# Kernel optimization log

Hardware: AMD Instinct MI355X
Metric: run time of the kernel (lower is better)

Reference implementation:

```python
import jax, jax.numpy as jnp
import numpy as np
from jax import lax

BN_INV = float(1.0 / np.sqrt(1.0 + 1e-5))  # BatchNorm eval: running_mean=0, running_var=1


def _block(x, w, b, g, beta, stride):
    # Conv3x3(stride, pad=1) -> BN(eval) -> ReLU -> MaxPool2
    x = lax.conv_general_dilated(x, w, (stride, stride), [(1, 1), (1, 1)],
                                 dimension_numbers=('NCHW', 'OIHW', 'NCHW'))
    x = x + b[None, :, None, None]
    x = x * (g * BN_INV)[None, :, None, None] + beta[None, :, None, None]
    x = jax.nn.relu(x)
    return lax.reduce_window(x, -jnp.inf, lax.max, (1, 1, 2, 2), (1, 1, 2, 2), 'VALID')


def _gru(x, wi, wh, bi, bh):
    # torch-style GRU, batch_first. x: (B, T, D)
    B = x.shape[0]
    H = wh.shape[1]

    def step(h, xt):
        gi = xt @ wi.T + bi
        gh = h @ wh.T + bh
        ir, iz, inn = jnp.split(gi, 3, axis=1)
        hr, hz, hn = jnp.split(gh, 3, axis=1)
        r = jax.nn.sigmoid(ir + hr)
        z = jax.nn.sigmoid(iz + hz)
        nn_ = jnp.tanh(inn + r * hn)
        h2 = (1.0 - z) * nn_ + z * h
        return h2, h2

    h0 = jnp.zeros((B, H), x.dtype)
    _, ys = lax.scan(step, h0, jnp.swapaxes(x, 0, 1))
    return jnp.swapaxes(ys, 0, 1)  # (B, T, H)


def setup_inputs() -> dict:
    key = jax.random.key(0)
    ks = jax.random.split(key, 32)
    rn = lambda i, shape, s: jax.random.normal(ks[i], shape, jnp.float32) * s
    inp = {
        'support': rn(0, (5, 5, 1, 224, 224), 1.0),
        'query': rn(1, (15, 1, 224, 224), 1.0),
        'conv_w1': rn(2, (32, 1, 3, 3), 0.3), 'conv_b1': rn(3, (32,), 0.1),
        'conv_w2': rn(4, (64, 32, 3, 3), 0.06), 'conv_b2': rn(5, (64,), 0.1),
        'conv_w3': rn(6, (128, 64, 3, 3), 0.04), 'conv_b3': rn(7, (128,), 0.1),
        'conv_w4': rn(8, (256, 128, 3, 3), 0.03), 'conv_b4': rn(9, (256,), 0.1),
        'bn_g1': 1.0 + rn(10, (32,), 0.05), 'bn_be1': rn(11, (32,), 0.05),
        'bn_g2': 1.0 + rn(12, (64,), 0.05), 'bn_be2': rn(13, (64,), 0.05),
        'bn_g3': 1.0 + rn(14, (128,), 0.05), 'bn_be3': rn(15, (128,), 0.05),
        'bn_g4': 1.0 + rn(16, (256,), 0.05), 'bn_be4': rn(17, (256,), 0.05),
        'att_w': rn(18, (64, 256), 0.06), 'att_b': rn(19, (64,), 0.05),
        'gru_wi0': rn(20, (384, 512), 0.04), 'gru_wh0': rn(21, (384, 128), 0.08),
        'gru_bi0': rn(22, (384,), 0.05), 'gru_bh0': rn(23, (384,), 0.05),
        'gru_wi1': rn(24, (384, 128), 0.08), 'gru_wh1': rn(25, (384, 128), 0.08),
        'gru_bi1': rn(26, (384,), 0.05), 'gru_bh1': rn(27, (384,), 0.05),
        'trans_w': rn(28, (1, 128), 0.08), 'trans_b': rn(29, (1,), 0.05),
    }
    return inp


def reference(support, query, conv_w1, conv_b1, conv_w2, conv_b2, conv_w3, conv_b3,
              conv_w4, conv_b4, bn_g1, bn_be1, bn_g2, bn_be2, bn_g3, bn_be3,
              bn_g4, bn_be4, att_w, att_b, gru_wi0, gru_wh0, gru_bi0, gru_bh0,
              gru_wi1, gru_wh1, gru_bi1, gru_bh1, trans_w, trans_b):
    n, k, c, w = support.shape[0], support.shape[1], support.shape[2], support.shape[3]
    qk = query.shape[0]

    def enc(x):
        x = _block(x, conv_w1, conv_b1, bn_g1, bn_be1, 2)
        x = _block(x, conv_w2, conv_b2, bn_g2, bn_be2, 1)
        x = _block(x, conv_w3, conv_b3, bn_g3, bn_be3, 1)
        x = _block(x, conv_w4, conv_b4, bn_g4, bn_be4, 1)
        B, F_, H_, W_ = x.shape
        return x.reshape(B, F_, H_ * W_).transpose(0, 2, 1)  # (B, seq, feat)

    hf = enc(support.reshape(n * k, c, w, w))  # (nk, S, f)
    qf = enc(query)                            # (qk, T, f)

    # ItemQueryAttention: score[q,s,t,u] = sum_h tanh(W(q_t) * W(h_u))
    Wq = qf @ att_w.T + att_b  # (qk, T, h)
    Wh = hf @ att_w.T + att_b  # (nk, S, h)
    scores = jnp.tanh(Wq[:, None, :, None, :] * Wh[None, :, None, :, :]).sum(-1)  # (qk,nk,T,S)
    att = jax.nn.softmax(scores, axis=3)
    attended = jnp.einsum('qsTS,sSf->qsTf', att, hf)  # (qk, nk, T, f)

    T_, f = qf.shape[1], qf.shape[2]
    qrep = jnp.broadcast_to(qf[:, None], (qk, n * k, T_, f))
    x = jnp.concatenate([attended, qrep], axis=-1).reshape(qk * n * k, T_, 2 * f)

    h = _gru(x, gru_wi0, gru_wh0, gru_bi0, gru_bh0)
    h = _gru(h, gru_wi1, gru_wh1, gru_bi1, gru_bh1)

    logits = (h[:, -1, :] @ trans_w.T + trans_b).reshape(qk, n, k).sum(axis=2)  # (qk, n)
    return jax.nn.log_softmax(logits, axis=1)
```

## Files before the change

kernel.cpp:

```cpp
#include <hip/hip_runtime.h>
#include <hip/hip_bf16.h>
#include <math.h>

typedef unsigned short u16;
typedef unsigned int u32;
typedef __attribute__((ext_vector_type(8))) short bf16x8v;
typedef __attribute__((ext_vector_type(4))) float f32x4;

constexpr int NS = 25, NQ = 15, NB = 40;
constexpr int B3 = 375;
constexpr int T49 = 49;
constexpr float BN_INV = 0.9999950000374997f;

constexpr size_t A1H_OFF    = 0;
constexpr size_t A1L_OFF    = 8028160;
constexpr size_t X2_OFF     = 16056320;
constexpr size_t P2H_OFF    = 48168960;
constexpr size_t P2L_OFF    = 52183040;
constexpr size_t X3_OFF     = 0;
constexpr size_t P3H_OFF    = 56197120;
constexpr size_t P3L_OFF    = 58204160;
constexpr size_t X4_OFF     = 0;
constexpr size_t FEATTH_OFF = 60211200;
constexpr size_t FEATTL_OFF = 61214720;
constexpr size_t PROJ_OFF   = 0;
constexpr size_t ATTH_OFF   = 16056320;
constexpr size_t ATTL_OFF   = 25464320;
constexpr size_t GI_OFF     = 62218240;
constexpr size_t Y0H_OFF    = 0;
constexpr size_t Y0L_OFF    = 4704000;
constexpr size_t HFIN_OFF   = 90442240;
constexpr size_t WBH_OFF    = 91027456;
constexpr size_t WBL_OFF    = 92325888;
constexpr size_t W2_E = 0;
constexpr size_t W3_E = 18432;
constexpr size_t W4_E = 92160;
constexpr size_t AW_E = 387072;
constexpr size_t WI0_E = 403456;
constexpr size_t WI1_E = 600064;
constexpr int CVT_N = 649216;

static __device__ __forceinline__ u16 f2b(float f) {
  __hip_bfloat16 h = __float2bfloat16(f);
  return *reinterpret_cast<u16*>(&h);
}
static __device__ __forceinline__ float b2f(u16 u) {
  return __uint_as_float((u32)u << 16);
}
constexpr float LOG2E = 1.4426950408889634f;
static __device__ __forceinline__ float fsigmoid(float x) {
  return __builtin_amdgcn_rcpf(1.f + __builtin_amdgcn_exp2f(-x * LOG2E));
}
static __device__ __forceinline__ float ftanh(float x) {
  return 1.f - 2.f * __builtin_amdgcn_rcpf(__builtin_amdgcn_exp2f(x * (2.f * LOG2E)) + 1.f);
}
static __device__ __forceinline__ void split8(const float* v, u32* hp, u32* lp) {
  u16 h[8], l[8];
#pragma unroll
  for (int j = 0; j < 8; ++j) {
    const u16 hb = f2b(v[j]);
    h[j] = hb;
    l[j] = f2b(v[j] - b2f(hb));
  }
#pragma unroll
  for (int j = 0; j < 4; ++j) {
    hp[j] = (u32)h[2 * j] | ((u32)h[2 * j + 1] << 16);
    lp[j] = (u32)l[2 * j] | ((u32)l[2 * j + 1] << 16);
  }
}

__global__ void cvt_all(const float* __restrict__ cw2, const float* __restrict__ cw3,
                        const float* __restrict__ cw4, const float* __restrict__ aw,
                        const float* __restrict__ wi0, const float* __restrict__ wi1,
                        u16* __restrict__ oh, u16* __restrict__ ol) {
  const int i = blockIdx.x * 256 + threadIdx.x;
  if (i >= CVT_N) return;
  float v;
  if (i < (int)W3_E) {
    const int l = i, oc = l / 288, rem = l - oc * 288, e = rem >> 5, ic = rem & 31;
    v = cw2[((size_t)(oc * 32 + ic) * 3 + e / 3) * 3 + e % 3];
  } else if (i < (int)W4_E) {
    const int l = i - (int)W3_E, oc = l / 576, rem = l - oc * 576, e = rem >> 6, ic = rem & 63;
    v = cw3[((size_t)(oc * 64 + ic) * 3 + e / 3) * 3 + e % 3];
  } else if (i < (int)AW_E) {
    const int l = i - (int)W4_E, oc = l / 1152, rem = l - oc * 1152, e = rem >> 7, ic = rem & 127;
    v = cw4[((size_t)(oc * 128 + ic) * 3 + e / 3) * 3 + e % 3];
  } else if (i < (int)WI0_E) {
    v = aw[i - (int)AW_E];
  } else if (i < (int)WI1_E) {
    v = wi0[i - (int)WI0_E];
  } else {
    v = wi1[i - (int)WI1_E];
  }
  const u16 h = f2b(v);
  oh[i] = h;
  ol[i] = f2b(v - b2f(h));
}

__global__ __launch_bounds__(256) void conv1_pool(
    const float* __restrict__ support, const float* __restrict__ query,
    const float* __restrict__ w1, const float* __restrict__ cb1,
    const float* __restrict__ g1, const float* __restrict__ be1,
    u16* __restrict__ outh, u16* __restrict__ outl) {
  __shared__ float wl[288], scl[32], shl[32], cbl[32];
  const int tid = threadIdx.x;
  for (int l = tid; l < 288; l += 256) wl[l] = w1[l];
  if (tid < 32) { scl[tid] = g1[tid] * BN_INV; shl[tid] = be1[tid]; cbl[tid] = cb1[tid]; }
  __syncthreads();
  const int oc = tid & 31;
  const int p = blockIdx.x * 8 + (tid >> 5);
  const int ox = p % 56, oy = (p / 56) % 56, b = p / 3136;
  const float* in_b = (b < NS) ? (support + (size_t)b * 50176)
                               : (query + (size_t)(b - NS) * 50176);
  const int iy0 = 4 * oy - 1, ix0 = 4 * ox - 1;
  float pat[5][5];
#pragma unroll
  for (int dy = 0; dy < 5; ++dy) {
    const int iy = iy0 + dy;
#pragma unroll
    for (int dx = 0; dx < 5; ++dx) {
      const int ix = ix0 + dx;
      pat[dy][dx] = (iy >= 0 && iy < 224 && ix >= 0 && ix < 224)
                        ? in_b[(size_t)iy * 224 + ix] : 0.f;
    }
  }
  const float* wp = &wl[oc * 9];
  float mx = 0.f;
#pragma unroll
  for (int py = 0; py < 2; ++py)
#pragma unroll
    for (int px = 0; px < 2; ++px) {
      float acc = 0.f;
#pragma unroll
      for (int ky = 0; ky < 3; ++ky)
#pragma unroll
        for (int kx = 0; kx < 3; ++kx)
          acc += pat[2 * py + ky][2 * px + kx] * wp[ky * 3 + kx];
      float v = (acc + cbl[oc]) * scl[oc] + shl[oc];
      mx = fmaxf(mx, v);
    }
  const u16 h = f2b(mx);
  outh[(size_t)p * 32 + oc] = h;
  outl[(size_t)p * 32 + oc] = f2b(mx - b2f(h));
}

__global__ void maxpool2_split(const float* __restrict__ X, u16* __restrict__ Yh,
                               u16* __restrict__ Yl, int Bn, int H, int W, int C) {
  const int OH = H >> 1, OW = W >> 1;
  const int cpr = C >> 2;
  const int chunks = Bn * OH * OW * cpr;
  for (int i = blockIdx.x * blockDim.x + threadIdx.x; i < chunks;
       i += gridDim.x * blockDim.x) {
    const int c4 = i % cpr, m = i / cpr;
    const int ox = m % OW, oy = (m / OW) % OH, b = m / (OW * OH);
    const size_t base = (((size_t)b * H + 2 * oy) * W + 2 * ox) * C + (c4 << 2);
    const float4 r0 = *(const float4*)&X[base];
    const float4 r1 = *(const float4*)&X[base + C];
    const float4 r2 = *(const float4*)&X[base + (size_t)W * C];
    const float4 r3 = *(const float4*)&X[base + (size_t)W * C + C];
    float o[4];
    o[0] = fmaxf(fmaxf(r0.x, r1.x), fmaxf(r2.x, r3.x));
    o[1] = fmaxf(fmaxf(r0.y, r1.y), fmaxf(r2.y, r3.y));
    o[2] = fmaxf(fmaxf(r0.z, r1.z), fmaxf(r2.z, r3.z));
    o[3] = fmaxf(fmaxf(r0.w, r1.w), fmaxf(r2.w, r3.w));
    u16 hh[4], ll[4];
#pragma unroll
    for (int j = 0; j < 4; ++j) {
      hh[j] = f2b(o[j]);
      ll[j] = f2b(o[j] - b2f(hh[j]));
    }
    const size_t off = (size_t)m * C + (c4 << 2);
    uint2 vh, vl;
    vh.x = (u32)hh[0] | ((u32)hh[1] << 16); vh.y = (u32)hh[2] | ((u32)hh[3] << 16);
    vl.x = (u32)ll[0] | ((u32)ll[1] << 16); vl.y = (u32)ll[2] | ((u32)ll[3] << 16);
    *(uint2*)&Yh[off] = vh;
    *(uint2*)&Yl[off] = vl;
  }
}

template <int AMODE, int EPI>
__global__ __launch_bounds__(256) void sgemm(
    const u16* __restrict__ Ah, const u16* __restrict__ Al,
    const u16* __restrict__ A2h, const u16* __restrict__ A2l, int M, int K,
    const u16* __restrict__ Bh, const u16* __restrict__ Bl,
    const float* __restrict__ p0, const float* __restrict__ p1,
    const float* __restrict__ p2, float* __restrict__ Cout, int ldc,
    int H, int W, int IC, int icb) {
  __shared__ u16 Ash[64][72], Asl[64][72];
  __shared__ u16 Bsh[64][72], Bsl[64][72];
  const int tid = threadIdx.x;
  const int lane = tid & 63, wv = tid >> 6;
  const int wy = wv >> 1, wx = wv & 1;
  const int n0 = blockIdx.x * 64, m0 = blockIdx.y * 64;
  f32x4 acc[2][2] = {{{0, 0, 0, 0}, {0, 0, 0, 0}}, {{0, 0, 0, 0}, {0, 0, 0, 0}}};
  for (int k0 = 0; k0 < K; k0 += 64) {
#pragma unroll
    for (int s = 0; s < 2; ++s) {
      const int cc = s * 256 + tid;
      const int row = cc >> 3, kc = (cc & 7) << 3;
      const int gm = m0 + row, gk = k0 + kc;
      uint4 vh = {0u, 0u, 0u, 0u}, vl = {0u, 0u, 0u, 0u};
      if (AMODE == 0) {
        if (gm < M && gk < K) {
          const size_t idx = (size_t)gm * K + gk;
          vh = *(const uint4*)&Ah[idx];
          vl = *(const uint4*)&Al[idx];
        }
      } else if (AMODE == 1) {
        if (gm < M) {
          size_t idx;
          const u16 *ph_, *pl_;
          if (gk < 256) {
            idx = (size_t)gm * 256 + gk; ph_ = Ah; pl_ = Al;
          } else {
            const int b = gm / T49, t = gm % T49, q = b / NS;
            idx = (((size_t)(NS + q) * T49 + t) << 8) + (gk - 256);
            ph_ = A2h; pl_ = A2l;
          }
          vh = *(const uint4*)&ph_[idx];
          vl = *(const uint4*)&pl_[idx];
        }
      } else {
        if (gm < M && gk < K) {
          const int ox = gm % W, t_ = gm / W;
          const int oy = t_ % H, b = t_ / H;
          const int e = gk >> icb, ic = gk & (IC - 1);
          const int ky = e / 3, kx = e - 3 * (e / 3);
          const int iy = oy + ky - 1, ix = ox + kx - 1;
          if (iy >= 0 && iy < H && ix >= 0 && ix < W) {
            const size_t idx = (((size_t)b * H + iy) * W + ix) * IC + ic;
            vh = *(const uint4*)&Ah[idx];
            vl = *(const uint4*)&Al[idx];
          }
        }
      }
      *(uint4*)&Ash[row][kc] = vh;
      *(uint4*)&Asl[row][kc] = vl;
    }
#pragma unroll
    for (int s = 0; s < 2; ++s) {
      const int cc = s * 256 + tid;
      const int row = cc >> 3, kc = (cc & 7) << 3;
      const int gk = k0 + kc;
      uint4 vh = {0u, 0u, 0u, 0u}, vl = {0u, 0u, 0u, 0u};
      if (gk < K) {
        vh = *(const uint4*)&Bh[(size_t)(n0 + row) * K + gk];
        vl = *(const uint4*)&Bl[(size_t)(n0 + row) * K + gk];
      }
      *(uint4*)&Bsh[row][kc] = vh;
      *(uint4*)&Bsl[row][kc] = vl;
    }
    __syncthreads();
#pragma unroll
    for (int kk = 0; kk < 64; kk += 32) {
      const int ko = kk + ((lane >> 4) << 3);
      const int ra0 = wy * 32 + (lane & 15), ra1 = ra0 + 16;
      const int rb0 = wx * 32 + (lane & 15), rb1 = rb0 + 16;
      bf16x8v a0h = *(const bf16x8v*)&Ash[ra0][ko];
      bf16x8v a1h = *(const bf16x8v*)&Ash[ra1][ko];
      bf16x8v b0h = *(const bf16x8v*)&Bsh[rb0][ko];
      bf16x8v b1h = *(const bf16x8v*)&Bsh[rb1][ko];
      bf16x8v a0l = *(const bf16x8v*)&Asl[ra0][ko];
      bf16x8v a1l = *(const bf16x8v*)&Asl[ra1][ko];
      bf16x8v b0l = *(const bf16x8v*)&Bsl[rb0][ko];
      bf16x8v b1l = *(const bf16x8v*)&Bsl[rb1][ko];
      acc[0][0] = __builtin_amdgcn_mfma_f32_16x16x32_bf16(a0h, b0h, acc[0][0], 0, 0, 0);
      acc[0][1] = __builtin_amdgcn_mfma_f32_16x16x32_bf16(a0h, b1h, acc[0][1], 0, 0, 0);
      acc[1][0] = __builtin_amdgcn_mfma_f32_16x16x32_bf16(a1h, b0h, acc[1][0], 0, 0, 0);
      acc[1][1] = __builtin_amdgcn_mfma_f32_16x16x32_bf16(a1h, b1h, acc[1][1], 0, 0, 0);
      acc[0][0] = __builtin_amdgcn_mfma_f32_16x16x32_bf16(a0h, b0l, acc[0][0], 0, 0, 0);
      acc[0][1] = __builtin_amdgcn_mfma_f32_16x16x32_bf16(a0h, b1l, acc[0][1], 0, 0, 0);
      acc[1][0] = __builtin_amdgcn_mfma_f32_16x16x32_bf16(a1h, b0l, acc[1][0], 0, 0, 0);
      acc[1][1] = __builtin_amdgcn_mfma_f32_16x16x32_bf16(a1h, b1l, acc[1][1], 0, 0, 0);
      acc[0][0] = __builtin_amdgcn_mfma_f32_16x16x32_bf16(a0l, b0h, acc[0][0], 0, 0, 0);
      acc[0][1] = __builtin_amdgcn_mfma_f32_16x16x32_bf16(a0l, b1h, acc[0][1], 0, 0, 0);
      acc[1][0] = __builtin_amdgcn_mfma_f32_16x16x32_bf16(a1l, b0h, acc[1][0], 0, 0, 0);
      acc[1][1] = __builtin_amdgcn_mfma_f32_16x16x32_bf16(a1l, b1h, acc[1][1], 0, 0, 0);
    }
    __syncthreads();
  }
#pragma unroll
  for (int r = 0; r < 2; ++r) {
#pragma unroll
    for (int cI = 0; cI < 2; ++cI) {
      const int gn = n0 + wx * 32 + cI * 16 + (lane & 15);
      float sc0 = 0.f, sh0 = 0.f;
      if (EPI == 0) { sc0 = p1[gn] * BN_INV; sh0 = p2[gn]; }
#pragma unroll
      for (int i = 0; i < 4; ++i) {
        const int gm = m0 + wy * 32 + r * 16 + ((lane >> 4) << 2) + i;
        if (gm >= M) continue;
        const float a = acc[r][cI][i];
        if (EPI == 0) {
          Cout[(size_t)gm * ldc + gn] = fmaxf((a + p0[gn]) * sc0 + sh0, 0.f);
        } else {
          Cout[(size_t)gm * ldc + gn] = a + p0[gn];
        }
      }
    }
  }
}

__global__ __launch_bounds__(384) void attention_f32(
    const float* __restrict__ proj, const u16* __restrict__ featTh,
    const u16* __restrict__ featTl, u16* __restrict__ atth,
    u16* __restrict__ attl) {
  __shared__ float WqT[64][9];
  __shared__ float WhT[64][51];
  __shared__ float sc[7][64];
  const int bid = blockIdx.x;
  const int qs = bid / 7, tg = bid - 7 * qs;
  const int q = qs / NS, s = qs - NS * q;
  const int tid = threadIdx.x;
  const float* pq = proj + ((size_t)(NS + q) * T49 + tg * 7) * 64;
  const float* ph = proj + (size_t)s * T49 * 64;
  for (int l = tid; l < 7 * 64; l += 384) WqT[l & 63][l >> 6] = pq[l];
  for (int l = tid; l < T49 * 64; l += 384) WhT[l & 63][l >> 6] = ph[l];
  __syncthreads();
  constexpr float C2LOG2E = 2.8853900817779268f;
  if (tid < 343) {
    const int tl = tid / 49, u = tid - 49 * tl;
    float a0 = 0.f, a1 = 0.f, a2 = 0.f, a3 = 0.f;
#pragma unroll
    for (int h = 0; h < 64; h += 4) {
      const float p0 = WqT[h + 0][tl] * WhT[h + 0][u];
      const float p1 = WqT[h + 1][tl] * WhT[h + 1][u];
      const float p2 = WqT[h + 2][tl] * WhT[h + 2][u];
      const float p3 = WqT[h + 3][tl] * WhT[h + 3][u];
      a0 += 1.f - 2.f * __builtin_amdgcn_rcpf(__builtin_amdgcn_exp2f(p0 * C2LOG2E) + 1.f);
      a1 += 1.f - 2.f * __builtin_amdgcn_rcpf(__builtin_amdgcn_exp2f(p1 * C2LOG2E) + 1.f);
      a2 += 1.f - 2.f * __builtin_amdgcn_rcpf(__builtin_amdgcn_exp2f(p2 * C2LOG2E) + 1.f);
      a3 += 1.f - 2.f * __builtin_amdgcn_rcpf(__builtin_amdgcn_exp2f(p3 * C2LOG2E) + 1.f);
    }
    sc[tl][u] = (a0 + a1) + (a2 + a3);
  }
  __syncthreads();
  if (tid < 56) {
    const int t = tid >> 3, g = tid & 7;
    float m = -3.4e38f;
    for (int u = g; u < T49; u += 8) m = fmaxf(m, sc[t][u]);
    m = fmaxf(m, __shfl_xor(m, 4));
    m = fmaxf(m, __shfl_xor(m, 2));
    m = fmaxf(m, __shfl_xor(m, 1));
    float ssum = 0.f;
    for (int u = g; u < T49; u += 8) {
      const float e = __builtin_amdgcn_exp2f((sc[t][u] - m) * LOG2E);
      sc[t][u] = e; ssum += e;
    }
    ssum += __shfl_xor(ssum, 4);
    ssum += __shfl_xor(ssum, 2);
    ssum += __shfl_xor(ssum, 1);
    const float inv = 1.f / ssum;
    for (int u = g; u < T49; u += 8) sc[t][u] *= inv;
  }
  __syncthreads();
  if (tid < 256) {
    const u16* fsh = featTh + (size_t)s * T49 * 256;
    const u16* fsl = featTl + (size_t)s * T49 * 256;
    const size_t obase = ((size_t)qs * T49 + tg * 7) * 256;
    float acc[7] = {0.f, 0.f, 0.f, 0.f, 0.f, 0.f, 0.f};
    for (int u = 0; u < T49; ++u) {
      const float v = b2f(fsh[u * 256 + tid]) + b2f(fsl[u * 256 + tid]);
#pragma unroll
      for (int i = 0; i < 7; ++i) acc[i] += sc[i][u] * v;
    }
#pragma unroll
    for (int i = 0; i < 7; ++i) {
      const float a = acc[i];
      const u16 h = f2b(a);
      atth[obase + (size_t)i * 256 + tid] = h;
      attl[obase + (size_t)i * 256 + tid] = f2b(a - b2f(h));
    }
  }
}

constexpr int SPB = 8;
__global__ __launch_bounds__(512) void gru_mfma(
    const float* __restrict__ gi,
    const float* __restrict__ wh,
    const float* __restrict__ bh,
    u16* __restrict__ yh, u16* __restrict__ yl,
    float* __restrict__ hfin,
    int store_all) {
  __shared__ u16 hah[16][136];
  __shared__ float ghs[SPB][384];
  __shared__ float hfl[SPB][128];
  const int tid = threadIdx.x;
  const int lane = tid & 63, wv = tid >> 6;
  const int r0 = blockIdx.x * SPB;
  bf16x8v Bhr[3][4], Blr[3][4];
#pragma unroll
  for (int f = 0; f < 3; ++f) {
    const int n = (wv * 3 + f) * 16 + (lane & 15);
#pragma unroll
    for (int kk = 0; kk < 4; ++kk) {
      const int k = kk * 32 + ((lane >> 4) << 3);
      const float* p = wh + (size_t)n * 128 + k;
      float v[8];
      *(float4*)&v[0] = *(const float4*)p;
      *(float4*)&v[4] = *(const float4*)(p + 4);
      u32 hp[4], lp[4];
      split8(v, hp, lp);
      Bhr[f][kk] = *(bf16x8v*)hp;
      Blr[f][kk] = *(bf16x8v*)lp;
    }
  }
  const int row0 = tid >> 7, j0 = tid & 127;
  const int row1 = (512 + tid) >> 7, j1 = tid & 127;
  int sq0 = r0 + row0; if (sq0 >= B3) sq0 = B3 - 1;
  int sq1 = r0 + row1; if (sq1 >= B3) sq1 = B3 - 1;
  const float bhr0 = bh[j0], bhz0 = bh[128 + j0], bhn0 = bh[256 + j0];
  const float bhr1 = bh[j1], bhz1 = bh[128 + j1], bhn1 = bh[256 + j1];
  const float* gib0 = gi + (size_t)sq0 * T49 * 384;
  const float* gib1 = gi + (size_t)sq1 * T49 * 384;
  for (int i = tid; i < 16 * 136; i += 512) hah[i / 136][i % 136] = 0;
  for (int i = tid; i < SPB * 128; i += 512) hfl[i >> 7][i & 127] = 0.f;
  __syncthreads();
  const int ar = lane & 15, ko = (lane >> 4) << 3;
  float xr0c = gib0[j0], xz0c = gib0[128 + j0], xn0c = gib0[256 + j0];
  float xr1c = gib1[j1], xz1c = gib1[128 + j1], xn1c = gib1[256 + j1];
  for (int t = 0; t < T49; ++t) {
    const int tn = (t + 1 < T49) ? t + 1 : t;
    const float* g0n = gib0 + (size_t)tn * 384;
    const float* g1n = gib1 + (size_t)tn * 384;
    const float xr0n = g0n[j0], xz0n = g0n[128 + j0], xn0n = g0n[256 + j0];
    const float xr1n = g1n[j1], xz1n = g1n[128 + j1], xn1n = g1n[256 + j1];
    bf16x8v Ah[4];
#pragma unroll
    for (int kk = 0; kk < 4; ++kk)
      Ah[kk] = *(const bf16x8v*)&hah[ar][kk * 32 + ko];
#pragma unroll
    for (int f = 0; f < 3; ++f) {
      f32x4 acc = {0, 0, 0, 0};
#pragma unroll
      for (int kk = 0; kk < 4; ++kk)
        acc = __builtin_amdgcn_mfma_f32_16x16x32_bf16(Ah[kk], Bhr[f][kk], acc, 0, 0, 0);
#pragma unroll
      for (int kk = 0; kk < 4; ++kk)
        acc = __builtin_amdgcn_mfma_f32_16x16x32_bf16(Ah[kk], Blr[f][kk], acc, 0, 0, 0);
      const int nc = (wv * 3 + f) * 16 + (lane & 15);
      const int rb = (lane >> 4) << 2;
      if (rb < SPB) {
#pragma unroll
        for (int i = 0; i < 4; ++i) ghs[rb + i][nc] = acc[i];
      }
    }
    __syncthreads();
    {
      const float r_ = fsigmoid(xr0c + ghs[row0][j0] + bhr0);
      const float z_ = fsigmoid(xz0c + ghs[row0][128 + j0] + bhz0);
      const float n_ = ftanh(xn0c + r_ * (ghs[row0][256 + j0] + bhn0));
      const float hn = (1.f - z_) * n_ + z_ * hfl[row0][j0];
      hfl[row0][j0] = hn;
      const u16 hb = f2b(hn);
      hah[row0][j0] = hb;
      if (r0 + row0 < B3) {
        if (store_all) {
          const size_t o = ((size_t)(r0 + row0) * T49 + t) * 128 + j0;
          yh[o] = hb;
          yl[o] = f2b(hn - b2f(hb));
        } else if (t == T49 - 1) {
          hfin[(size_t)(r0 + row0) * 128 + j0] = hn;
        }
      }
    }
    {
      const float r_ = fsigmoid(xr1c + ghs[row1][j1] + bhr1);
      const float z_ = fsigmoid(xz1c + ghs[row1][128 + j1] + bhz1);
      const float n_ = ftanh(xn1c + r_ * (ghs[row1][256 + j1] + bhn1));
      const float hn = (1.f - z_) * n_ + z_ * hfl[row1][j1];
      hfl[row1][j1] = hn;
      const u16 hb = f2b(hn);
      hah[row1][j1] = hb;
      if (r0 + row1 < B3) {
        if (store_all) {
          const size_t o = ((size_t)(r0 + row1) * T49 + t) * 128 + j1;
          yh[o] = hb;
          yl[o] = f2b(hn - b2f(hb));
        } else if (t == T49 - 1) {
          hfin[(size_t)(r0 + row1) * 128 + j1] = hn;
        }
      }
    }
    __syncthreads();
    xr0c = xr0n; xz0c = xz0n; xn0c = xn0n;
    xr1c = xr1n; xz1c = xz1n; xn1c = xn1n;
  }
}

__global__ __launch_bounds__(512) void head_kernel(
    const float* __restrict__ hf, const float* __restrict__ tw,
    const float* __restrict__ tb, float* __restrict__ out) {
  __shared__ float lg[B3];
  const int tid = threadIdx.x;
  if (tid < B3) {
    const float* h = hf + (size_t)tid * 128;
    float acc = tb[0];
    for (int k = 0; k < 128; ++k) acc += h[k] * tw[k];
    lg[tid] = acc;
  }
  __syncthreads();
  if (tid < NQ) {
    float cls[5];
#pragma unroll
    for (int n = 0; n < 5; ++n) {
      float s = 0.f;
#pragma unroll
      for (int k = 0; k < 5; ++k) s += lg[tid * 25 + n * 5 + k];
      cls[n] = s;
    }
    float m = cls[0];
#pragma unroll
    for (int n = 1; n < 5; ++n) m = fmaxf(m, cls[n]);
    float se = 0.f;
#pragma unroll
    for (int n = 0; n < 5; ++n) se += expf(cls[n] - m);
    const float lse = m + logf(se);
#pragma unroll
    for (int n = 0; n < 5; ++n) out[tid * 5 + n] = cls[n] - lse;
  }
}

extern "C" void kernel_launch(void* const* d_in, const int* in_sizes, int n_in,
                              void* d_out, int out_size, void* d_ws,
                              size_t ws_size, hipStream_t stream) {
  (void)in_sizes; (void)n_in; (void)out_size; (void)ws_size;
  const float* support = (const float*)d_in[0];
  const float* query   = (const float*)d_in[1];
  const float* cw1 = (const float*)d_in[2];  const float* cb1 = (const float*)d_in[3];
  const float* cw2 = (const float*)d_in[4];  const float* cb2 = (const float*)d_in[5];
  const float* cw3 = (const float*)d_in[6];  const float* cb3 = (const float*)d_in[7];
  const float* cw4 = (const float*)d_in[8];  const float* cb4 = (const float*)d_in[9];
  const float* g1  = (const float*)d_in[10]; const float* be1 = (const float*)d_in[11];
  const float* g2  = (const float*)d_in[12]; const float* be2 = (const float*)d_in[13];
  const float* g3  = (const float*)d_in[14]; const float* be3 = (const float*)d_in[15];
  const float* g4  = (const float*)d_in[16]; const float* be4 = (const float*)d_in[17];
  const float* aw  = (const float*)d_in[18]; const float* ab  = (const float*)d_in[19];
  const float* wi0 = (const float*)d_in[20]; const float* wh0 = (const float*)d_in[21];
  const float* bi0 = (const float*)d_in[22]; const float* bh0 = (const float*)d_in[23];
  const float* wi1 = (const float*)d_in[24]; const float* wh1 = (const float*)d_in[25];
  const float* bi1 = (const float*)d_in[26]; const float* bh1 = (const float*)d_in[27];
  const float* tw  = (const float*)d_in[28]; const float* tb  = (const float*)d_in[29];

  char* ws = (char*)d_ws;
  float* out = (float*)d_out;
  u16* A1H    = (u16*)(ws + A1H_OFF);
  u16* A1L    = (u16*)(ws + A1L_OFF);
  float* X2   = (float*)(ws + X2_OFF);
  u16* P2H    = (u16*)(ws + P2H_OFF);
  u16* P2L    = (u16*)(ws + P2L_OFF);
  float* X3   = (float*)(ws + X3_OFF);
  u16* P3H    = (u16*)(ws + P3H_OFF);
  u16* P3L    = (u16*)(ws + P3L_OFF);
  float* X4   = (float*)(ws + X4_OFF);
  u16* FEATTH = (u16*)(ws + FEATTH_OFF);
  u16* FEATTL = (u16*)(ws + FEATTL_OFF);
  float* PROJ = (float*)(ws + PROJ_OFF);
  u16* ATTH   = (u16*)(ws + ATTH_OFF);
  u16* ATTL   = (u16*)(ws + ATTL_OFF);
  float* GI   = (float*)(ws + GI_OFF);
  u16* Y0H    = (u16*)(ws + Y0H_OFF);
  u16* Y0L    = (u16*)(ws + Y0L_OFF);
  float* HFIN = (float*)(ws + HFIN_OFF);
  u16* WBH = (u16*)(ws + WBH_OFF);
  u16* WBL = (u16*)(ws + WBL_OFF);

  cvt_all<<<(CVT_N + 255) / 256, 256, 0, stream>>>(cw2, cw3, cw4, aw, wi0, wi1, WBH, WBL);

  conv1_pool<<<15680, 256, 0, stream>>>(support, query, cw1, cb1, g1, be1, A1H, A1L);
  sgemm<2, 0><<<dim3(1, 1960), 256, 0, stream>>>(
      A1H, A1L, nullptr, nullptr, 125440, 288, WBH + W2_E, WBL + W2_E,
      cb2, g2, be2, X2, 64, 56, 56, 32, 5);
  maxpool2_split<<<1960, 256, 0, stream>>>(X2, P2H, P2L, NB, 56, 56, 64);
  sgemm<2, 0><<<dim3(2, 490), 256, 0, stream>>>(
      P2H, P2L, nullptr, nullptr, 31360, 576, WBH + W3_E, WBL + W3_E,
      cb3, g3, be3, X3, 128, 28, 28, 64, 6);
  maxpool2_split<<<980, 256, 0, stream>>>(X3, P3H, P3L, NB, 28, 28, 128);
  sgemm<2, 0><<<dim3(4, 123), 256, 0, stream>>>(
      P3H, P3L, nullptr, nullptr, 7840, 1152, WBH + W4_E, WBL + W4_E,
      cb4, g4, be4, X4, 256, 14, 14, 128, 7);
  maxpool2_split<<<490, 256, 0, stream>>>(X4, FEATTH, FEATTL, NB, 14, 14, 256);

  sgemm<0, 1><<<dim3(1, 31), 256, 0, stream>>>(
      FEATTH, FEATTL, nullptr, nullptr, NB * T49, 256, WBH + AW_E, WBL + AW_E,
      ab, nullptr, nullptr, PROJ, 64, 0, 0, 0, 0);
  attention_f32<<<B3 * 7, 384, 0, stream>>>(PROJ, FEATTH, FEATTL, ATTH, ATTL);

  sgemm<1, 1><<<dim3(6, 288), 256, 0, stream>>>(
      ATTH, ATTL, FEATTH, FEATTL, B3 * T49, 512, WBH + WI0_E, WBL + WI0_E,
      bi0, nullptr, nullptr, GI, 384, 0, 0, 0, 0);
  gru_mfma<<<47, 512, 0, stream>>>(GI, wh0, bh0, Y0H, Y0L, nullptr, 1);
  sgemm<0, 1><<<dim3(6, 288), 256, 0, stream>>>(
      Y0H, Y0L, nullptr, nullptr, B3 * T49, 128, WBH + WI1_E, WBL + WI1_E,
      bi1, nullptr, nullptr, GI, 384, 0, 0, 0, 0);
  gru_mfma<<<47, 512, 0, stream>>>(GI, wh1, bh1, nullptr, nullptr, HFIN, 0);

  head_kernel<<<1, 512, 0, stream>>>(HFIN, tw, tb, out);
}
```

Before: 368.6 us.

## Precompute query half of GRU input projection once per query and broadcast

Result: no change. 368.1 us (-0.1%).

```diff
diff --git a/kernel.cpp b/kernel.cpp
--- a/kernel.cpp
+++ b/kernel.cpp
@@ -24,6 +24,7 @@
 constexpr size_t FEATTH_OFF = 60211200;
 constexpr size_t FEATTL_OFF = 61214720;
 constexpr size_t PROJ_OFF   = 0;
+constexpr size_t QG_OFF     = 1048576;
 constexpr size_t ATTH_OFF   = 16056320;
 constexpr size_t ATTL_OFF   = 25464320;
 constexpr size_t GI_OFF     = 62218240;
@@ -31,14 +32,17 @@
 constexpr size_t Y0L_OFF    = 4704000;
 constexpr size_t HFIN_OFF   = 90442240;
 constexpr size_t WBH_OFF    = 91027456;
-constexpr size_t WBL_OFF    = 92325888;
+constexpr size_t WBL_OFF    = 92719104;
 constexpr size_t W2_E = 0;
 constexpr size_t W3_E = 18432;
 constexpr size_t W4_E = 92160;
 constexpr size_t AW_E = 387072;
 constexpr size_t WI0_E = 403456;
 constexpr size_t WI1_E = 600064;
-constexpr int CVT_N = 649216;
+constexpr int    CVT_N = 649216;
+constexpr size_t WI0A_E = 649216;
+constexpr size_t WI0B_E = 747520;
+constexpr int    CVT_N2 = 845824;
 
 static __device__ __forceinline__ u16 f2b(float f) {
   __hip_bfloat16 h = __float2bfloat16(f);
@@ -74,7 +78,7 @@
                         const float* __restrict__ wi0, const float* __restrict__ wi1,
                         u16* __restrict__ oh, u16* __restrict__ ol) {
   const int i = blockIdx.x * 256 + threadIdx.x;
-  if (i >= CVT_N) return;
+  if (i >= CVT_N2) return;
   float v;
   if (i < (int)W3_E) {
     const int l = i, oc = l / 288, rem = l - oc * 288, e = rem >> 5, ic = rem & 31;
@@ -89,8 +93,14 @@
     v = aw[i - (int)AW_E];
   } else if (i < (int)WI1_E) {
     v = wi0[i - (int)WI0_E];
+  } else if (i < CVT_N) {
+    v = wi1[i - (int)WI1_E];
+  } else if (i < (int)WI0B_E) {
+    const int l = i - (int)WI0A_E, j = l >> 8, k = l & 255;
+    v = wi0[(size_t)j * 512 + k];
   } else {
-    v = wi1[i - (int)WI1_E];
+    const int l = i - (int)WI0B_E, j = l >> 8, k = l & 255;
+    v = wi0[(size_t)j * 512 + 256 + k];
   }
   const u16 h = f2b(v);
   oh[i] = h;
@@ -205,20 +215,6 @@
           const size_t idx = (size_t)gm * K + gk;
           vh = *(const uint4*)&Ah[idx];
           vl = *(const uint4*)&Al[idx];
-        }
-      } else if (AMODE == 1) {
-        if (gm < M) {
-          size_t idx;
-          const u16 *ph_, *pl_;
-          if (gk < 256) {
-            idx = (size_t)gm * 256 + gk; ph_ = Ah; pl_ = Al;
-          } else {
-            const int b = gm / T49, t = gm % T49, q = b / NS;
-            idx = (((size_t)(NS + q) * T49 + t) << 8) + (gk - 256);
-            ph_ = A2h; pl_ = A2l;
-          }
-          vh = *(const uint4*)&ph_[idx];
-          vl = *(const uint4*)&pl_[idx];
         }
       } else {
         if (gm < M && gk < K) {
@@ -293,8 +289,11 @@
         const float a = acc[r][cI][i];
         if (EPI == 0) {
           Cout[(size_t)gm * ldc + gn] = fmaxf((a + p0[gn]) * sc0 + sh0, 0.f);
+        } else if (EPI == 1) {
+          Cout[(size_t)gm * ldc + gn] = a + p0[gn];
         } else {
-          Cout[(size_t)gm * ldc + gn] = a + p0[gn];
+          const int b3 = gm / T49, q = b3 / NS, t = gm - b3 * T49;
+          Cout[(size_t)gm * ldc + gn] = a + p1[(size_t)(q * T49 + t) * 384 + gn];
         }
       }
     }
@@ -556,6 +555,7 @@
   u16* FEATTH = (u16*)(ws + FEATTH_OFF);
   u16* FEATTL = (u16*)(ws + FEATTL_OFF);
   float* PROJ = (float*)(ws + PROJ_OFF);
+  float* QG   = (float*)(ws + QG_OFF);
   u16* ATTH   = (u16*)(ws + ATTH_OFF);
   u16* ATTL   = (u16*)(ws + ATTL_OFF);
   float* GI   = (float*)(ws + GI_OFF);
@@ -565,7 +565,7 @@
   u16* WBH = (u16*)(ws + WBH_OFF);
   u16* WBL = (u16*)(ws + WBL_OFF);
 
-  cvt_all<<<(CVT_N + 255) / 256, 256, 0, stream>>>(cw2, cw3, cw4, aw, wi0, wi1, WBH, WBL);
+  cvt_all<<<(CVT_N2 + 255) / 256, 256, 0, stream>>>(cw2, cw3, cw4, aw, wi0, wi1, WBH, WBL);
 
   conv1_pool<<<15680, 256, 0, stream>>>(support, query, cw1, cb1, g1, be1, A1H, A1L);
   sgemm<2, 0><<<dim3(1, 1960), 256, 0, stream>>>(
@@ -581,14 +581,19 @@
       cb4, g4, be4, X4, 256, 14, 14, 128, 7);
   maxpool2_split<<<490, 256, 0, stream>>>(X4, FEATTH, FEATTL, NB, 14, 14, 256);
 
+  sgemm<0, 1><<<dim3(6, 12), 256, 0, stream>>>(
+      FEATTH + (size_t)NS * T49 * 256, FEATTL + (size_t)NS * T49 * 256,
+      nullptr, nullptr, NQ * T49, 256, WBH + WI0B_E, WBL + WI0B_E,
+      bi0, nullptr, nullptr, QG, 384, 0, 0, 0, 0);
+
   sgemm<0, 1><<<dim3(1, 31), 256, 0, stream>>>(
       FEATTH, FEATTL, nullptr, nullptr, NB * T49, 256, WBH + AW_E, WBL + AW_E,
       ab, nullptr, nullptr, PROJ, 64, 0, 0, 0, 0);
   attention_f32<<<B3 * 7, 384, 0, stream>>>(PROJ, FEATTH, FEATTL, ATTH, ATTL);
 
-  sgemm<1, 1><<<dim3(6, 288), 256, 0, stream>>>(
-      ATTH, ATTL, FEATTH, FEATTL, B3 * T49, 512, WBH + WI0_E, WBL + WI0_E,
-      bi0, nullptr, nullptr, GI, 384, 0, 0, 0, 0);
+  sgemm<0, 2><<<dim3(6, 288), 256, 0, stream>>>(
+      ATTH, ATTL, nullptr, nullptr, B3 * T49, 256, WBH + WI0A_E, WBL + WI0A_E,
+      nullptr, QG, nullptr, GI, 384, 0, 0, 0, 0);
   gru_mfma<<<47, 512, 0, stream>>>(GI, wh0, bh0, Y0H, Y0L, nullptr, 1);
   sgemm<0, 1><<<dim3(6, 288), 256, 0, stream>>>(
       Y0H, Y0L, nullptr, nullptr, B3 * T49, 128, WBH + WI1_E, WBL + WI1_E,
```
